# Performance work log

Measured on AMD Instinct MI355X. Metric: run time of the kernel, lower is better.

Reference implementation:

```python
import jax, jax.numpy as jnp
import numpy as np

B, H, W, C = 8, 64, 64, 512
G = 32  # num_groups
EPS = 1e-5


def group_norm(x, scale, bias):
    b, h, w, c = x.shape
    xg = x.reshape(b, h, w, G, c // G)
    mean = jnp.mean(xg, axis=(1, 2, 4), keepdims=True)
    var = jnp.var(xg, axis=(1, 2, 4), keepdims=True)
    xg = (xg - mean) / jnp.sqrt(var + EPS)
    x = xg.reshape(b, h, w, c)
    return x * scale + bias


def conv1x1(x, w, b):
    # NHWC 1x1 conv == channel matmul
    return jnp.einsum('bhwc,cd->bhwd', x, w) + b


def setup_inputs() -> dict:
    key = jax.random.key(0)
    ks = jax.random.split(key, 10)
    init = lambda k, shape: jax.random.normal(k, shape, dtype=jnp.float32) * (1.0 / np.sqrt(C))
    return {
        'x': jax.random.normal(ks[0], (B, H, W, C), dtype=jnp.float32),
        'gn_scale': jnp.ones((C,), dtype=jnp.float32),
        'gn_bias': jnp.zeros((C,), dtype=jnp.float32),
        'wq': init(ks[1], (C, C)), 'bq': jnp.zeros((C,), jnp.float32),
        'wk': init(ks[2], (C, C)), 'bk': jnp.zeros((C,), jnp.float32),
        'wv': init(ks[3], (C, C)), 'bv': jnp.zeros((C,), jnp.float32),
        'wo': init(ks[4], (C, C)), 'bo': jnp.zeros((C,), jnp.float32),
    }


def reference(x, gn_scale, gn_bias, wq, bq, wk, bk, wv, bv, wo, bo):
    h = group_norm(x, gn_scale, gn_bias)
    q = conv1x1(h, wq, bq)
    k = conv1x1(h, wk, bk)
    v = conv1x1(h, wv, bv)
    b, hh, ww, c = h.shape
    n = hh * ww
    q = q.reshape(b, n, c)
    k = k.reshape(b, n, c)
    v = v.reshape(b, n, c)
    scores = jnp.einsum('bqc,bkc->bqk', q, k) * (c ** -0.5)
    attn = jax.nn.softmax(scores, axis=-1)
    out = jnp.einsum('bqk,bkc->bqc', attn, v).reshape(b, hh, ww, c)
    out = conv1x1(out, wo, bo)
    return out + x
```

## Files before the change

### kernel.cpp

```cpp
#include <hip/hip_runtime.h>

typedef __bf16 bfx8 __attribute__((ext_vector_type(8)));
typedef __bf16 bfx4 __attribute__((ext_vector_type(4)));
typedef float  f32x4 __attribute__((ext_vector_type(4)));

#define MFMA16(a,b,c) __builtin_amdgcn_mfma_f32_16x16x32_bf16((a),(b),(c),0,0,0)

static constexpr int BATCH = 8;
static constexpr int NTOK  = 4096;
static constexpr int CH    = 512;
static constexpr float GN_EPS = 1e-5f;
static constexpr float ATT_SCALE = 0.044194173824159216f;

__global__ __launch_bounds__(256)
void prep_weights(const float* __restrict__ wq, const float* __restrict__ wk,
                  const float* __restrict__ wv, const float* __restrict__ wo,
                  const float* __restrict__ bq, const float* __restrict__ bk,
                  const float* __restrict__ bv,
                  __bf16* __restrict__ wqkvT, __bf16* __restrict__ woT,
                  float* __restrict__ bqkv)
{
    __shared__ __bf16 t[32][36];
    const int z  = blockIdx.z;
    const float* src = (z == 0) ? wq : (z == 1) ? wk : (z == 2) ? wv : wo;
    const int c0 = blockIdx.x * 32, n0 = blockIdx.y * 32;
    const int tid = threadIdx.x;
    const int r = tid >> 3, c4 = (tid & 7) * 4;

    f32x4 in = *(const f32x4*)&src[(size_t)(c0 + r) * 512 + n0 + c4];
    bfx4 tv;
#pragma unroll
    for (int i = 0; i < 4; ++i) tv[i] = (__bf16)in[i];
    *(bfx4*)&t[r][c4] = tv;
    __syncthreads();
    bfx4 o;
#pragma unroll
    for (int i = 0; i < 4; ++i) o[i] = t[c4 + i][r];
    if (z < 3)
        *(bfx4*)&wqkvT[((size_t)(z * 512 + n0 + r)) * 512 + c0 + c4] = o;
    else
        *(bfx4*)&woT[((size_t)(n0 + r)) * 512 + c0 + c4] = o;

    if (z < 3 && blockIdx.x == 0 && blockIdx.y == 0) {
        const float* bs = (z == 0) ? bq : (z == 1) ? bk : bv;
        bqkv[z * 512 + tid]       = bs[tid];
        bqkv[z * 512 + tid + 256] = bs[tid + 256];
    }
}

__global__ __launch_bounds__(256)
void gn_stats(const float* __restrict__ x, const float* __restrict__ gs,
              const float* __restrict__ gb,
              float* __restrict__ scA, float* __restrict__ biA)
{
    const int g = blockIdx.x, b = blockIdx.y;
    const int tid = threadIdx.x;
    const int half = tid & 1;
    const size_t base = (size_t)b * NTOK * CH + g * 16 + half * 8;

    float sum = 0.f, sumsq = 0.f;
    for (int i = tid; i < 2 * NTOK; i += 256) {
        const int s = i >> 1;
        f32x4 v0 = *(const f32x4*)&x[base + (size_t)s * CH];
        f32x4 v1 = *(const f32x4*)&x[base + (size_t)s * CH + 4];
#pragma unroll
        for (int j = 0; j < 4; ++j) {
            sum += v0[j] + v1[j];
            sumsq += v0[j] * v0[j] + v1[j] * v1[j];
        }
    }
#pragma unroll
    for (int o = 32; o; o >>= 1) { sum += __shfl_down(sum, o); sumsq += __shfl_down(sumsq, o); }
    __shared__ float red[8];
    __shared__ float stats[2];
    const int w = tid >> 6;
    if ((tid & 63) == 0) { red[w] = sum; red[4 + w] = sumsq; }
    __syncthreads();
    if (tid == 0) {
        float s1 = red[0] + red[1] + red[2] + red[3];
        float s2 = red[4] + red[5] + red[6] + red[7];
        float mean = s1 * (1.f / 65536.f);
        float var  = s2 * (1.f / 65536.f) - mean * mean;
        stats[0] = mean; stats[1] = rsqrtf(var + GN_EPS);
    }
    __syncthreads();
    if (tid < 16) {
        const int ch = g * 16 + tid;
        const float sc = gs[ch] * stats[1];
        scA[b * 512 + ch] = sc;
        biA[b * 512 + ch] = gb[ch] - stats[0] * sc;
    }
}

__global__ __launch_bounds__(256)
void gemm_qkv(const float* __restrict__ x, const float* __restrict__ scA,
              const float* __restrict__ biA, const __bf16* __restrict__ Bt,
              const float* __restrict__ bias,
              __bf16* __restrict__ qk, __bf16* __restrict__ vT)
{
    const int bm = blockIdx.x * 128, bn = blockIdx.y * 128;
    const int tid = threadIdx.x;
    const int w = tid >> 6, lane = tid & 63, quad = lane >> 4, l15 = lane & 15;
    const int wm = (w >> 1) * 64, wn = (w & 1) * 64;
    const int brow = bm >> 12;

    __shared__ __bf16 sAB[2][128][40];

    f32x4 acc[4][4];
#pragma unroll
    for (int i = 0; i < 4; ++i)
#pragma unroll
        for (int j = 0; j < 4; ++j) acc[i][j] = (f32x4){0.f, 0.f, 0.f, 0.f};

    const int sr = tid >> 2, scol = (tid & 3) * 8;
    for (int k0 = 0; k0 < 512; k0 += 32) {
        __syncthreads();
        {
            const float* scp = scA + brow * 512 + k0 + scol;
            const float* bip = biA + brow * 512 + k0 + scol;
            f32x4 s0v = *(const f32x4*)&scp[0], s1v = *(const f32x4*)&scp[4];
            f32x4 b0v = *(const f32x4*)&bip[0], b1v = *(const f32x4*)&bip[4];
            f32x4 xa0 = *(const f32x4*)&x[(size_t)(bm + sr) * 512 + k0 + scol];
            f32x4 xa1 = *(const f32x4*)&x[(size_t)(bm + sr) * 512 + k0 + scol + 4];
            f32x4 xb0 = *(const f32x4*)&x[(size_t)(bm + sr + 64) * 512 + k0 + scol];
            f32x4 xb1 = *(const f32x4*)&x[(size_t)(bm + sr + 64) * 512 + k0 + scol + 4];
            bfx8 ha, hb;
#pragma unroll
            for (int j = 0; j < 4; ++j) {
                ha[j]     = (__bf16)(xa0[j] * s0v[j] + b0v[j]);
                ha[4 + j] = (__bf16)(xa1[j] * s1v[j] + b1v[j]);
                hb[j]     = (__bf16)(xb0[j] * s0v[j] + b0v[j]);
                hb[4 + j] = (__bf16)(xb1[j] * s1v[j] + b1v[j]);
            }
            *(bfx8*)&sAB[0][sr][scol]      = ha;
            *(bfx8*)&sAB[0][sr + 64][scol] = hb;
        }
        *(bfx8*)&sAB[1][sr][scol]      = *(const bfx8*)&Bt[(size_t)(bn + sr) * 512 + k0 + scol];
        *(bfx8*)&sAB[1][sr + 64][scol] = *(const bfx8*)&Bt[(size_t)(bn + sr + 64) * 512 + k0 + scol];
        __syncthreads();
        bfx8 af[4], bfr[4];
#pragma unroll
        for (int mi = 0; mi < 4; ++mi) af[mi]  = *(const bfx8*)&sAB[0][wm + mi * 16 + l15][quad * 8];
#pragma unroll
        for (int ni = 0; ni < 4; ++ni) bfr[ni] = *(const bfx8*)&sAB[1][wn + ni * 16 + l15][quad * 8];
#pragma unroll
        for (int mi = 0; mi < 4; ++mi)
#pragma unroll
            for (int ni = 0; ni < 4; ++ni)
                acc[mi][ni] = MFMA16(af[mi], bfr[ni], acc[mi][ni]);
    }

    if (blockIdx.y < 8) {
#pragma unroll
        for (int ni = 0; ni < 4; ++ni) {
            const int col = bn + wn + ni * 16 + l15;
            const float bv = bias[col];
#pragma unroll
            for (int mi = 0; mi < 4; ++mi)
#pragma unroll
                for (int rr = 0; rr < 4; ++rr) {
                    const int row = bm + wm + mi * 16 + quad * 4 + rr;
                    qk[(size_t)row * 1024 + col] = (__bf16)(acc[mi][ni][rr] + bv);
                }
        }
    } else {
        const int vch0 = bn - 1024;
        const int tokbase = bm & 4095;
        __bf16* tb = &sAB[0][0][0];
        __syncthreads();
#pragma unroll
        for (int chunk = 0; chunk < 2; ++chunk) {
            if ((w & 1) == chunk) {
#pragma unroll
                for (int ni = 0; ni < 4; ++ni) {
                    const int chc = ni * 16 + l15;
                    const float bv = bias[bn + chunk * 64 + chc];
#pragma unroll
                    for (int mi = 0; mi < 4; ++mi)
#pragma unroll
                        for (int rr = 0; rr < 4; ++rr) {
                            const int tok = wm + mi * 16 + quad * 4 + rr;
                            tb[chc * 136 + tok] = (__bf16)(acc[mi][ni][rr] + bv);
                        }
                }
            }
            __syncthreads();
            {
                const int chn = tid >> 2, t0 = (tid & 3) * 32;
                const size_t gb0 =
                    ((size_t)(brow * 512 + vch0 + chunk * 64 + chn)) * 4096 + tokbase;
#pragma unroll
                for (int u = 0; u < 4; ++u)
                    *(bfx8*)&vT[gb0 + t0 + u * 8] = *(const bfx8*)&tb[chn * 136 + t0 + u * 8];
            }
            __syncthreads();
        }
    }
}

__global__ __launch_bounds__(512, 2)
void attn_fused(const __bf16* __restrict__ qk, const __bf16* __restrict__ vT,
                const __bf16* __restrict__ woT, const float* __restrict__ bo,
                const float* __restrict__ x, float* __restrict__ out)
{
    const int bb = blockIdx.y;
    const int q0 = blockIdx.x * 128;
    const int tid = threadIdx.x;
    const int w = tid >> 6, lane = tid & 63, quad = lane >> 4, l15 = lane & 15;

    __shared__ __attribute__((aligned(16))) unsigned char smem[85520];
    __bf16 (*Ks)[520] = (__bf16(*)[520])smem;
    __bf16 (*Vs)[40]  = (__bf16(*)[40])(smem + 33280);
    __bf16 (*Ph)[40]  = (__bf16(*)[40])(smem + 74240);
    float* abuf  = (float*)(smem + 84480);
    float* lbuf  = (float*)(smem + 84992);
    int*   rflag = (int*)(smem + 85504);
    __bf16 (*Obuf)[520] = (__bf16(*)[520])smem;

    bfx8 qf[16];
    {
        const __bf16* qptr = qk + ((size_t)(bb * NTOK + q0 + w * 16 + l15)) * 1024;
#pragma unroll
        for (int kk = 0; kk < 16; ++kk)
            qf[kk] = *(const bfx8*)&qptr[kk * 32 + quad * 8];
    }

    f32x4 oacc[4][8];
#pragma unroll
    for (int i = 0; i < 4; ++i)
#pragma unroll
        for (int j = 0; j < 8; ++j) oacc[i][j] = (f32x4){0.f, 0.f, 0.f, 0.f};
    float mcur = -1e30f, lcur = 0.f;

    const __bf16* kbase = qk + ((size_t)(bb * NTOK) + w * 4) * 1024 + 512 + lane * 8;
    const __bf16* vbase = vT + ((size_t)(bb * 512 + w * 64 + (lane >> 2))) * 4096 + (lane & 3) * 8;

    bfx8 kreg[4], vreg[4];
#pragma unroll
    for (int u = 0; u < 4; ++u) kreg[u] = *(const bfx8*)&kbase[u * 1024];
#pragma unroll
    for (int u = 0; u < 4; ++u) vreg[u] = *(const bfx8*)&vbase[(size_t)u * 16 * 4096];

    const int rh = (w & 1) * 64;
    const int cq = (w >> 1) * 128;

    for (int kt = 0; kt < NTOK / 32; ++kt) {
#pragma unroll
        for (int u = 0; u < 4; ++u) *(bfx8*)&Ks[w * 4 + u][lane * 8] = kreg[u];
#pragma unroll
        for (int u = 0; u < 4; ++u)
            *(bfx8*)&Vs[w * 64 + u * 16 + (lane >> 2)][(lane & 3) * 8] = vreg[u];
        __syncthreads();

        {
            const int ktn = (kt < NTOK / 32 - 1) ? kt + 1 : kt;
            const __bf16* kp = kbase + (size_t)ktn * 32 * 1024;
            const __bf16* vp = vbase + ktn * 32;
#pragma unroll
            for (int u = 0; u < 4; ++u) kreg[u] = *(const bfx8*)&kp[u * 1024];
#pragma unroll
            for (int u = 0; u < 4; ++u) vreg[u] = *(const bfx8*)&vp[(size_t)u * 16 * 4096];
        }

        f32x4 s0 = (f32x4){0.f, 0.f, 0.f, 0.f}, s1 = (f32x4){0.f, 0.f, 0.f, 0.f};
#pragma unroll
        for (int kk = 0; kk < 16; ++kk) {
            bfx8 kb0 = *(const bfx8*)&Ks[l15][kk * 32 + quad * 8];
            bfx8 kb1 = *(const bfx8*)&Ks[16 + l15][kk * 32 + quad * 8];
            s0 = MFMA16(kb0, qf[kk], s0);
            s1 = MFMA16(kb1, qf[kk], s1);
        }

        {
            float mx = -1e30f;
#pragma unroll
            for (int i = 0; i < 4; ++i) {
                s0[i] *= ATT_SCALE; s1[i] *= ATT_SCALE;
                mx = fmaxf(mx, fmaxf(s0[i], s1[i]));
            }
            mx = fmaxf(mx, __shfl_xor(mx, 16));
            mx = fmaxf(mx, __shfl_xor(mx, 32));
            const float mnew = fmaxf(mcur, mx);
            const float al = __expf(mcur - mnew);
            float ps = 0.f;
            bfx4 pl0, pl1;
#pragma unroll
            for (int i = 0; i < 4; ++i) {
                float p = __expf(s0[i] - mnew); ps += p; pl0[i] = (__bf16)p;
            }
#pragma unroll
            for (int i = 0; i < 4; ++i) {
                float p = __expf(s1[i] - mnew); ps += p; pl1[i] = (__bf16)p;
            }
            ps += __shfl_xor(ps, 16);
            ps += __shfl_xor(ps, 32);
            lcur = lcur * al + ps;
            mcur = mnew;
            *(bfx4*)&Ph[w * 16 + l15][quad * 4]      = pl0;
            *(bfx4*)&Ph[w * 16 + l15][16 + quad * 4] = pl1;
            if (quad == 0) abuf[w * 16 + l15] = al;
            if (__ballot(al != 1.0f)) { if (lane == 0) rflag[kt & 1] = 1; }
            if (tid == 0) rflag[(kt + 1) & 1] = 0;
        }
        __syncthreads();

        if (rflag[kt & 1]) {
#pragma unroll
            for (int mt = 0; mt < 4; ++mt)
#pragma unroll
                for (int r = 0; r < 4; ++r) {
                    const float al = abuf[rh + mt * 16 + quad * 4 + r];
#pragma unroll
                    for (int ct = 0; ct < 8; ++ct) oacc[mt][ct][r] *= al;
                }
        }
        bfx8 pa[4];
#pragma unroll
        for (int mt = 0; mt < 4; ++mt)
            pa[mt] = *(const bfx8*)&Ph[rh + mt * 16 + l15][quad * 8];
#pragma unroll
        for (int ct = 0; ct < 8; ++ct) {
            bfx8 vb = *(const bfx8*)&Vs[cq + ct * 16 + l15][quad * 8];
#pragma unroll
            for (int mt = 0; mt < 4; ++mt)
                oacc[mt][ct] = MFMA16(pa[mt], vb, oacc[mt][ct]);
        }
        __syncthreads();
    }

    if (quad == 0) lbuf[w * 16 + l15] = lcur;

#pragma unroll
    for (int h = 0; h < 2; ++h) {
        __syncthreads();
        if ((w & 1) == h) {
#pragma unroll
            for (int mt = 0; mt < 4; ++mt)
#pragma unroll
                for (int r = 0; r < 4; ++r) {
                    const int rl = mt * 16 + quad * 4 + r;
                    const float linv = 1.f / lbuf[h * 64 + rl];
#pragma unroll
                    for (int ct = 0; ct < 8; ++ct)
                        Obuf[rl][cq + ct * 16 + l15] = (__bf16)(oacc[mt][ct][r] * linv);
                }
        }
        __syncthreads();

        const int rs  = (w & 3) * 16;
        const int nt0 = (w >> 2) * 16;
        bfx8 af2[16];
#pragma unroll
        for (int k0 = 0; k0 < 16; ++k0)
            af2[k0] = *(const bfx8*)&Obuf[rs + l15][k0 * 32 + quad * 8];
#pragma unroll 4
        for (int nt = 0; nt < 16; ++nt) {
            f32x4 a2 = (f32x4){0.f, 0.f, 0.f, 0.f};
#pragma unroll
            for (int k0 = 0; k0 < 16; ++k0) {
                bfx8 wb = *(const bfx8*)&woT[(size_t)((nt0 + nt) * 16 + l15) * 512 + k0 * 32 + quad * 8];
                a2 = MFMA16(af2[k0], wb, a2);
            }
            const int col = (nt0 + nt) * 16 + l15;
            const float bv = bo[col];
#pragma unroll
            for (int rr = 0; rr < 4; ++rr) {
                const size_t idx =
                    ((size_t)(bb * NTOK + q0 + h * 64 + rs + quad * 4 + rr)) * 512 + col;
                out[idx] = a2[rr] + bv + x[idx];
            }
        }
    }
}

extern "C" void kernel_launch(void* const* d_in, const int* in_sizes, int n_in,
                              void* d_out, int out_size, void* d_ws, size_t ws_size,
                              hipStream_t stream)
{
    const float* x  = (const float*)d_in[0];
    const float* gs = (const float*)d_in[1];
    const float* gb = (const float*)d_in[2];
    const float* wq = (const float*)d_in[3];
    const float* bq = (const float*)d_in[4];
    const float* wk = (const float*)d_in[5];
    const float* bk = (const float*)d_in[6];
    const float* wv = (const float*)d_in[7];
    const float* bv = (const float*)d_in[8];
    const float* wo = (const float*)d_in[9];
    const float* bo = (const float*)d_in[10];
    float* out = (float*)d_out;

    char* ws = (char*)d_ws;
    __bf16* qk    = (__bf16*)(ws);
    __bf16* vT    = (__bf16*)(ws + 67108864);
    __bf16* wqkvT = (__bf16*)(ws + 100663296);
    __bf16* woT   = (__bf16*)(ws + 102236160);
    float*  bqkv  = (float* )(ws + 102760448);
    float*  scA   = (float* )(ws + 102766592);
    float*  biA   = (float* )(ws + 102782976);

    prep_weights<<<dim3(16, 16, 4), 256, 0, stream>>>(wq, wk, wv, wo, bq, bk, bv,
                                                      wqkvT, woT, bqkv);
    gn_stats<<<dim3(32, BATCH), 256, 0, stream>>>(x, gs, gb, scA, biA);
    gemm_qkv<<<dim3(256, 12), 256, 0, stream>>>(x, scA, biA, wqkvT, bqkv, qk, vT);
    attn_fused<<<dim3(NTOK / 128, BATCH), 512, 0, stream>>>(qk, vT, woT, bo, x, out);
}
```

Baseline: 862.1 us.

## Double-buffer K/V via direct global-to-LDS loads with swizzled K and per-wave query rows

K and V tiles now go straight from global memory into LDS with global_load_lds. They are double-buffered, so the next tile is fetched while the current one is computed, replacing the register-staged prefetch. The K tile uses an XOR swizzle to avoid LDS bank conflicts. V is stored in an MFMA-friendly layout. Each wave now owns 16 query rows across all 512 output channels, so the shared alpha and flag buffers and one barrier per iteration go away. The cost is a larger LDS footprint (about 138 KB), which likely drops occupancy to one block per CU.

New measurement: 776.1 us. 1.11x faster.

```diff
diff --git a/kernel.cpp b/kernel.cpp
--- a/kernel.cpp
+++ b/kernel.cpp
@@ -11,6 +11,13 @@
 static constexpr int CH    = 512;
 static constexpr float GN_EPS = 1e-5f;
 static constexpr float ATT_SCALE = 0.044194173824159216f;
+
+__device__ __forceinline__ void gload16(const void* g, void* l)
+{
+    __builtin_amdgcn_global_load_lds(
+        (const __attribute__((address_space(1))) unsigned int*)g,
+        (__attribute__((address_space(3))) unsigned int*)l, 16, 0, 0);
+}
 
 __global__ __launch_bounds__(256)
 void prep_weights(const float* __restrict__ wq, const float* __restrict__ wk,
@@ -208,14 +215,11 @@
     const int tid = threadIdx.x;
     const int w = tid >> 6, lane = tid & 63, quad = lane >> 4, l15 = lane & 15;
 
-    __shared__ __attribute__((aligned(16))) unsigned char smem[85520];
-    __bf16 (*Ks)[520] = (__bf16(*)[520])smem;
-    __bf16 (*Vs)[40]  = (__bf16(*)[40])(smem + 33280);
-    __bf16 (*Ph)[40]  = (__bf16(*)[40])(smem + 74240);
-    float* abuf  = (float*)(smem + 84480);
-    float* lbuf  = (float*)(smem + 84992);
-    int*   rflag = (int*)(smem + 85504);
-    __bf16 (*Obuf)[520] = (__bf16(*)[520])smem;
+    __shared__ __attribute__((aligned(16))) unsigned char smem[141312];
+    __bf16 (*Ks)[32][512]      = (__bf16(*)[32][512])smem;
+    __bf16 (*Vs)[32][4][16][8] = (__bf16(*)[32][4][16][8])(smem + 65536);
+    __bf16 (*Ph)[40]           = (__bf16(*)[40])(smem + 131072);
+    __bf16 (*Obuf)[520]        = (__bf16(*)[520])smem;
 
     bfx8 qf[16];
     {
@@ -225,125 +229,110 @@
             qf[kk] = *(const bfx8*)&qptr[kk * 32 + quad * 8];
     }
 
-    f32x4 oacc[4][8];
-#pragma unroll
-    for (int i = 0; i < 4; ++i)
-#pragma unroll
-        for (int j = 0; j < 8; ++j) oacc[i][j] = (f32x4){0.f, 0.f, 0.f, 0.f};
+    f32x4 oacc[32];
+#pragma unroll
+    for (int i = 0; i < 32; ++i) oacc[i] = (f32x4){0.f, 0.f, 0.f, 0.f};
     float mcur = -1e30f, lcur = 0.f;
 
-    const __bf16* kbase = qk + ((size_t)(bb * NTOK) + w * 4) * 1024 + 512 + lane * 8;
-    const __bf16* vbase = vT + ((size_t)(bb * 512 + w * 64 + (lane >> 2))) * 4096 + (lane & 3) * 8;
-
-    bfx8 kreg[4], vreg[4];
-#pragma unroll
-    for (int u = 0; u < 4; ++u) kreg[u] = *(const bfx8*)&kbase[u * 1024];
-#pragma unroll
-    for (int u = 0; u < 4; ++u) vreg[u] = *(const bfx8*)&vbase[(size_t)u * 16 * 4096];
-
-    const int rh = (w & 1) * 64;
-    const int cq = (w >> 1) * 128;
-
-    for (int kt = 0; kt < NTOK / 32; ++kt) {
-#pragma unroll
-        for (int u = 0; u < 4; ++u) *(bfx8*)&Ks[w * 4 + u][lane * 8] = kreg[u];
-#pragma unroll
-        for (int u = 0; u < 4; ++u)
-            *(bfx8*)&Vs[w * 64 + u * 16 + (lane >> 2)][(lane & 3) * 8] = vreg[u];
-        __syncthreads();
-
-        {
-            const int ktn = (kt < NTOK / 32 - 1) ? kt + 1 : kt;
-            const __bf16* kp = kbase + (size_t)ktn * 32 * 1024;
-            const __bf16* vp = vbase + ktn * 32;
-#pragma unroll
-            for (int u = 0; u < 4; ++u) kreg[u] = *(const bfx8*)&kp[u * 1024];
-#pragma unroll
-            for (int u = 0; u < 4; ++u) vreg[u] = *(const bfx8*)&vp[(size_t)u * 16 * 4096];
+#pragma unroll
+    for (int u = 0; u < 4; ++u) {
+        const int r = w * 4 + u;
+        gload16(qk + ((size_t)(bb * NTOK + r)) * 1024 + 512 + ((lane ^ (r & 7)) * 8),
+                &Ks[0][r][0]);
+    }
+#pragma unroll
+    for (int u = 0; u < 4; ++u) {
+        const int g = w * 4 + u;
+        gload16(vT + ((size_t)(bb * 512 + g * 16 + (lane & 15))) * 4096 + (lane >> 4) * 8,
+                &Vs[0][g][0][0][0]);
+    }
+
+    const int NT = NTOK / 32;
+    int buf = 0;
+    for (int kt = 0; kt < NT; ++kt) {
+        __syncthreads();
+
+        if (kt + 1 < NT) {
+            const int kv1 = (kt + 1) * 32;
+            const int nb = buf ^ 1;
+#pragma unroll
+            for (int u = 0; u < 4; ++u) {
+                const int r = w * 4 + u;
+                gload16(qk + ((size_t)(bb * NTOK + kv1 + r)) * 1024 + 512 + ((lane ^ (r & 7)) * 8),
+                        &Ks[nb][r][0]);
+            }
+#pragma unroll
+            for (int u = 0; u < 4; ++u) {
+                const int g = w * 4 + u;
+                gload16(vT + ((size_t)(bb * 512 + g * 16 + (lane & 15))) * 4096 + kv1 + (lane >> 4) * 8,
+                        &Vs[nb][g][0][0][0]);
+            }
         }
 
         f32x4 s0 = (f32x4){0.f, 0.f, 0.f, 0.f}, s1 = (f32x4){0.f, 0.f, 0.f, 0.f};
 #pragma unroll
         for (int kk = 0; kk < 16; ++kk) {
-            bfx8 kb0 = *(const bfx8*)&Ks[l15][kk * 32 + quad * 8];
-            bfx8 kb1 = *(const bfx8*)&Ks[16 + l15][kk * 32 + quad * 8];
+            const int pc = (((kk * 4 + quad) ^ (l15 & 7)) * 8);
+            bfx8 kb0 = *(const bfx8*)&Ks[buf][l15][pc];
+            bfx8 kb1 = *(const bfx8*)&Ks[buf][16 + l15][pc];
             s0 = MFMA16(kb0, qf[kk], s0);
             s1 = MFMA16(kb1, qf[kk], s1);
         }
 
-        {
-            float mx = -1e30f;
-#pragma unroll
-            for (int i = 0; i < 4; ++i) {
-                s0[i] *= ATT_SCALE; s1[i] *= ATT_SCALE;
-                mx = fmaxf(mx, fmaxf(s0[i], s1[i]));
-            }
-            mx = fmaxf(mx, __shfl_xor(mx, 16));
-            mx = fmaxf(mx, __shfl_xor(mx, 32));
-            const float mnew = fmaxf(mcur, mx);
-            const float al = __expf(mcur - mnew);
-            float ps = 0.f;
-            bfx4 pl0, pl1;
-#pragma unroll
-            for (int i = 0; i < 4; ++i) {
-                float p = __expf(s0[i] - mnew); ps += p; pl0[i] = (__bf16)p;
-            }
-#pragma unroll
-            for (int i = 0; i < 4; ++i) {
-                float p = __expf(s1[i] - mnew); ps += p; pl1[i] = (__bf16)p;
-            }
-            ps += __shfl_xor(ps, 16);
-            ps += __shfl_xor(ps, 32);
-            lcur = lcur * al + ps;
-            mcur = mnew;
-            *(bfx4*)&Ph[w * 16 + l15][quad * 4]      = pl0;
-            *(bfx4*)&Ph[w * 16 + l15][16 + quad * 4] = pl1;
-            if (quad == 0) abuf[w * 16 + l15] = al;
-            if (__ballot(al != 1.0f)) { if (lane == 0) rflag[kt & 1] = 1; }
-            if (tid == 0) rflag[(kt + 1) & 1] = 0;
-        }
-        __syncthreads();
-
-        if (rflag[kt & 1]) {
-#pragma unroll
-            for (int mt = 0; mt < 4; ++mt)
-#pragma unroll
-                for (int r = 0; r < 4; ++r) {
-                    const float al = abuf[rh + mt * 16 + quad * 4 + r];
-#pragma unroll
-                    for (int ct = 0; ct < 8; ++ct) oacc[mt][ct][r] *= al;
-                }
-        }
-        bfx8 pa[4];
-#pragma unroll
-        for (int mt = 0; mt < 4; ++mt)
-            pa[mt] = *(const bfx8*)&Ph[rh + mt * 16 + l15][quad * 8];
-#pragma unroll
-        for (int ct = 0; ct < 8; ++ct) {
-            bfx8 vb = *(const bfx8*)&Vs[cq + ct * 16 + l15][quad * 8];
-#pragma unroll
-            for (int mt = 0; mt < 4; ++mt)
-                oacc[mt][ct] = MFMA16(pa[mt], vb, oacc[mt][ct]);
-        }
-        __syncthreads();
-    }
-
-    if (quad == 0) lbuf[w * 16 + l15] = lcur;
+        float mx = -1e30f;
+#pragma unroll
+        for (int i = 0; i < 4; ++i) {
+            s0[i] *= ATT_SCALE; s1[i] *= ATT_SCALE;
+            mx = fmaxf(mx, fmaxf(s0[i], s1[i]));
+        }
+        mx = fmaxf(mx, __shfl_xor(mx, 16));
+        mx = fmaxf(mx, __shfl_xor(mx, 32));
+        const float mnew = fmaxf(mcur, mx);
+        const float al = __expf(mcur - mnew);
+        float ps = 0.f;
+        bfx4 pl0, pl1;
+#pragma unroll
+        for (int i = 0; i < 4; ++i) { float p = __expf(s0[i] - mnew); ps += p; pl0[i] = (__bf16)p; }
+#pragma unroll
+        for (int i = 0; i < 4; ++i) { float p = __expf(s1[i] - mnew); ps += p; pl1[i] = (__bf16)p; }
+        ps += __shfl_xor(ps, 16);
+        ps += __shfl_xor(ps, 32);
+        lcur = lcur * al + ps;
+        mcur = mnew;
+
+        *(bfx4*)&Ph[w * 16 + l15][quad * 4]      = pl0;
+        *(bfx4*)&Ph[w * 16 + l15][16 + quad * 4] = pl1;
+
+        if (__any(al != 1.0f)) {
+#pragma unroll
+            for (int ct = 0; ct < 32; ++ct)
+#pragma unroll
+                for (int r = 0; r < 4; ++r) oacc[ct][r] *= al;
+        }
+
+        asm volatile("s_waitcnt lgkmcnt(0)" ::: "memory");
+        bfx8 pa = *(const bfx8*)&Ph[w * 16 + l15][quad * 8];
+
+#pragma unroll
+        for (int ct = 0; ct < 32; ++ct) {
+            bfx8 vb = *(const bfx8*)&Vs[buf][ct][quad][l15][0];
+            oacc[ct] = MFMA16(vb, pa, oacc[ct]);
+        }
+        buf ^= 1;
+    }
 
 #pragma unroll
     for (int h = 0; h < 2; ++h) {
         __syncthreads();
-        if ((w & 1) == h) {
-#pragma unroll
-            for (int mt = 0; mt < 4; ++mt)
-#pragma unroll
-                for (int r = 0; r < 4; ++r) {
-                    const int rl = mt * 16 + quad * 4 + r;
-                    const float linv = 1.f / lbuf[h * 64 + rl];
-#pragma unroll
-                    for (int ct = 0; ct < 8; ++ct)
-                        Obuf[rl][cq + ct * 16 + l15] = (__bf16)(oacc[mt][ct][r] * linv);
-                }
+        if ((w >> 2) == h) {
+            const float linv = 1.f / lcur;
+#pragma unroll
+            for (int ct = 0; ct < 32; ++ct) {
+                bfx4 ov;
+#pragma unroll
+                for (int r = 0; r < 4; ++r) ov[r] = (__bf16)(oacc[ct][r] * linv);
+                *(bfx4*)&Obuf[(w & 3) * 16 + l15][ct * 16 + quad * 4] = ov;
+            }
         }
         __syncthreads();
 
```
